# Performance work log

Hardware: AMD Instinct MI355X
Metric: run time of the kernel (lower is better)

Reference implementation:

```python
import jax, jax.numpy as jnp
import numpy as np

WIN = (9, 9)
EPS = float(np.power(np.e, -15))  # e^-15 threshold from original code


def _box_sum(x, win):
    kernel = jnp.ones((1, 1, win[0], win[1]), dtype=x.dtype)
    p = win[0] // 2
    return jax.lax.conv_general_dilated(
        x, kernel, window_strides=(1, 1), padding=[(p, p), (p, p)],
        dimension_numbers=("NCHW", "OIHW", "NCHW"))


def setup_inputs() -> dict:
    key = jax.random.key(0)
    k1, k2 = jax.random.split(key)
    B, C, H, W = 32, 1, 512, 512
    I = jax.random.normal(k1, (B, C, H, W), dtype=jnp.float32)
    J = jax.random.normal(k2, (B, C, H, W), dtype=jnp.float32)
    return {"I": I, "J": J}


def reference(I, J):
    win = WIN
    win_size = win[0] * win[1]
    I_sum = _box_sum(I, win)
    J_sum = _box_sum(J, win)
    I2_sum = _box_sum(I * I, win)
    J2_sum = _box_sum(J * J, win)
    IJ_sum = _box_sum(I * J, win)

    u_I = I_sum / win_size
    u_J = J_sum / win_size
    cross = IJ_sum - u_J * I_sum - u_I * J_sum + u_I * u_J * win_size
    I_var = I2_sum - 2 * u_I * I_sum + u_I * u_I * win_size
    J_var = J2_sum - 2 * u_J * J_sum + u_J * u_J * win_size

    non_zero = I_var * J_var > EPS
    cross = jnp.where(non_zero, cross, 1.0)
    I_var = jnp.where(non_zero, I_var, 1.0)
    J_var = jnp.where(non_zero, J_var, 1.0)

    cc = cross * cross / (I_var * J_var + EPS)
    return -1.0 * jnp.mean(cc, axis=(1, 2, 3)) + 1.0
```

## Files before the change

### kernel.cpp

```cpp
#include <hip/hip_runtime.h>


#define IMG_H 512
#define IMG_W 512
#define NBATCH 32
#define RPW 32
#define STRIPS_PER_IMG (IMG_H / RPW)
#define RING 10

typedef __attribute__((address_space(3))) void       lds_t;
typedef __attribute__((address_space(1))) const void glob_t;

__global__ __launch_bounds__(64, 1) void lcc_main(const float* __restrict__ I,
                                                  const float* __restrict__ J,
                                                  float* __restrict__ out) {
    __shared__ __align__(16) float ring[RING][1024];

    const int lane  = threadIdx.x;
    const int strip = blockIdx.x;
    const int b  = strip / STRIPS_PER_IMG;
    const int y0 = (strip % STRIPS_PER_IMG) * RPW;
    const int x0 = lane * 8;

    const float* __restrict__ Ib = I + (size_t)b * IMG_H * IMG_W;
    const float* __restrict__ Jb = J + (size_t)b * IMG_H * IMG_W;

    auto issue_row = [&](int y) {
        int slot = (y - y0 + 4) % RING;
        const float* gI = Ib + y * IMG_W;
        const float* gJ = Jb + y * IMG_W;
        float* lI = &ring[slot][0];
        float* lJ = &ring[slot][512];
        __builtin_amdgcn_global_load_lds((glob_t*)(gI +       lane * 4), (lds_t*)lI,         16, 0, 0);
        __builtin_amdgcn_global_load_lds((glob_t*)(gI + 256 + lane * 4), (lds_t*)(lI + 256), 16, 0, 0);
        __builtin_amdgcn_global_load_lds((glob_t*)(gJ +       lane * 4), (lds_t*)lJ,         16, 0, 0);
        __builtin_amdgcn_global_load_lds((glob_t*)(gJ + 256 + lane * 4), (lds_t*)(lJ + 256), 16, 0, 0);
    };

    float sI[8]  = {0.f,0.f,0.f,0.f,0.f,0.f,0.f,0.f};
    float sJ[8]  = {0.f,0.f,0.f,0.f,0.f,0.f,0.f,0.f};
    float sII[8] = {0.f,0.f,0.f,0.f,0.f,0.f,0.f,0.f};
    float sJJ[8] = {0.f,0.f,0.f,0.f,0.f,0.f,0.f,0.f};
    float sIJ[8] = {0.f,0.f,0.f,0.f,0.f,0.f,0.f,0.f};

    auto add_ld = [&](int y) {
        int slot = (y - y0 + 4) % RING;
        const float4* pI = reinterpret_cast<const float4*>(&ring[slot][x0]);
        const float4* pJ = reinterpret_cast<const float4*>(&ring[slot][512 + x0]);
        float4 i0 = pI[0], i1 = pI[1], j0 = pJ[0], j1 = pJ[1];
        float iv[8] = {i0.x,i0.y,i0.z,i0.w,i1.x,i1.y,i1.z,i1.w};
        float jv[8] = {j0.x,j0.y,j0.z,j0.w,j1.x,j1.y,j1.z,j1.w};
        #pragma unroll
        for (int c = 0; c < 8; ++c) {
            sI[c]  += iv[c];
            sJ[c]  += jv[c];
            sII[c]  = fmaf(iv[c], iv[c], sII[c]);
            sJJ[c]  = fmaf(jv[c], jv[c], sJJ[c]);
            sIJ[c]  = fmaf(iv[c], jv[c], sIJ[c]);
        }
    };
    auto sub_ld = [&](int y) {
        int slot = (y - y0 + 4) % RING;
        const float4* pI = reinterpret_cast<const float4*>(&ring[slot][x0]);
        const float4* pJ = reinterpret_cast<const float4*>(&ring[slot][512 + x0]);
        float4 i0 = pI[0], i1 = pI[1], j0 = pJ[0], j1 = pJ[1];
        float iv[8] = {i0.x,i0.y,i0.z,i0.w,i1.x,i1.y,i1.z,i1.w};
        float jv[8] = {j0.x,j0.y,j0.z,j0.w,j1.x,j1.y,j1.z,j1.w};
        #pragma unroll
        for (int c = 0; c < 8; ++c) {
            sI[c]  -= iv[c];
            sJ[c]  -= jv[c];
            sII[c]  = fmaf(-iv[c], iv[c], sII[c]);
            sJJ[c]  = fmaf(-jv[c], jv[c], sJJ[c]);
            sIJ[c]  = fmaf(-iv[c], jv[c], sIJ[c]);
        }
    };

    auto hsum = [&](const float (&s)[8], float (&h)[8]) {
        float w[16];
        #pragma unroll
        for (int c = 0; c < 8; ++c) w[4+c] = s[c];
        #pragma unroll
        for (int c = 0; c < 4; ++c) {
            float a = __shfl_up(s[4+c], 1);
            w[c] = lane ? a : 0.f;
            a = __shfl_down(s[c], 1);
            w[12+c] = (lane < 63) ? a : 0.f;
        }
        float acc = 0.f;
        #pragma unroll
        for (int i = 0; i < 9; ++i) acc += w[i];
        h[0] = acc;
        #pragma unroll
        for (int k = 1; k < 8; ++k) { acc += w[k+8] - w[k-1]; h[k] = acc; }
    };

    const int wy_lo = (y0 - 4 < 0) ? 0 : y0 - 4;
    const int wy_hi = y0 + 4;
    #pragma unroll 1
    for (int y = wy_lo; y <= wy_hi; ++y) issue_row(y);
    __builtin_amdgcn_s_waitcnt(0x3F70);
    #pragma unroll 1
    for (int y = wy_lo; y <= wy_hi; ++y) add_ld(y);

    const float inv81 = 1.0f / 81.0f;
    const float EPSV  = 3.0590232050182579e-07f;
    float local = 0.0f;

    #pragma unroll 1
    for (int r = 0; r < RPW; ++r) {
        const int t = y0 + r;

        const bool pf = (r + 1 < RPW) && (t + 5 < IMG_H);
        if (pf) {
            __builtin_amdgcn_s_waitcnt(0xC07F);
            issue_row(t + 5);
        }

        float hI[8], hJ[8], hII[8], hJJ[8], hIJ[8];
        hsum(sI,  hI);
        hsum(sJ,  hJ);
        hsum(sII, hII);
        hsum(sJJ, hJJ);
        hsum(sIJ, hIJ);

        #pragma unroll
        for (int k = 0; k < 8; ++k) {
            float cross = fmaf(hI[k] * hJ[k], -inv81, hIJ[k]);
            float Iv    = fmaf(hI[k] * hI[k], -inv81, hII[k]);
            float Jv    = fmaf(hJ[k] * hJ[k], -inv81, hJJ[k]);
            float p  = Iv * Jv;
            bool  nz = p > EPSV;
            float c2 = nz ? cross : 1.0f;
            float p2 = nz ? p : 1.0f;
            local += (c2 * c2) * __builtin_amdgcn_rcpf(p2 + EPSV);
        }

        if (r + 1 < RPW) {
            if (pf) __builtin_amdgcn_s_waitcnt(0x3F70);
            if (t + 5 < IMG_H) add_ld(t + 5);
            if (t - 4 >= 0)    sub_ld(t - 4);
        }
    }

    #pragma unroll
    for (int off = 32; off > 0; off >>= 1) local += __shfl_down(local, off);
    if (lane == 0)
        atomicAdd(out + b, fmaf(local, -1.0f / (float)(IMG_H * IMG_W),
                                1.0f / (float)STRIPS_PER_IMG));
}

extern "C" void kernel_launch(void* const* d_in, const int* in_sizes, int n_in,
                              void* d_out, int out_size, void* d_ws, size_t ws_size,
                              hipStream_t stream) {
    const float* I = (const float*)d_in[0];
    const float* J = (const float*)d_in[1];
    float* out = (float*)d_out;

    const int total_strips = NBATCH * STRIPS_PER_IMG;
    lcc_main<<<total_strips, 64, 0, stream>>>(I, J, out);
}
```

Before: 125.1 us.

## Replace LDS ring buffer with direct global loads and shorter strips

New measurement: 118.2 us. 1.06x faster.

```diff
diff --git a/kernel.cpp b/kernel.cpp
--- a/kernel.cpp
+++ b/kernel.cpp
@@ -4,18 +4,12 @@
 #define IMG_H 512
 #define IMG_W 512
 #define NBATCH 32
-#define RPW 32
+#define RPW 8
 #define STRIPS_PER_IMG (IMG_H / RPW)
-#define RING 10
 
-typedef __attribute__((address_space(3))) void       lds_t;
-typedef __attribute__((address_space(1))) const void glob_t;
-
-__global__ __launch_bounds__(64, 1) void lcc_main(const float* __restrict__ I,
+__global__ __launch_bounds__(64, 2) void lcc_main(const float* __restrict__ I,
                                                   const float* __restrict__ J,
                                                   float* __restrict__ out) {
-    __shared__ __align__(16) float ring[RING][1024];
-
     const int lane  = threadIdx.x;
     const int strip = blockIdx.x;
     const int b  = strip / STRIPS_PER_IMG;
@@ -25,16 +19,10 @@
     const float* __restrict__ Ib = I + (size_t)b * IMG_H * IMG_W;
     const float* __restrict__ Jb = J + (size_t)b * IMG_H * IMG_W;
 
-    auto issue_row = [&](int y) {
-        int slot = (y - y0 + 4) % RING;
-        const float* gI = Ib + y * IMG_W;
-        const float* gJ = Jb + y * IMG_W;
-        float* lI = &ring[slot][0];
-        float* lJ = &ring[slot][512];
-        __builtin_amdgcn_global_load_lds((glob_t*)(gI +       lane * 4), (lds_t*)lI,         16, 0, 0);
-        __builtin_amdgcn_global_load_lds((glob_t*)(gI + 256 + lane * 4), (lds_t*)(lI + 256), 16, 0, 0);
-        __builtin_amdgcn_global_load_lds((glob_t*)(gJ +       lane * 4), (lds_t*)lJ,         16, 0, 0);
-        __builtin_amdgcn_global_load_lds((glob_t*)(gJ + 256 + lane * 4), (lds_t*)(lJ + 256), 16, 0, 0);
+    auto load_row = [&](int y, float4& i0, float4& i1, float4& j0, float4& j1) {
+        const float4* pI = reinterpret_cast<const float4*>(Ib + (size_t)y * IMG_W + x0);
+        const float4* pJ = reinterpret_cast<const float4*>(Jb + (size_t)y * IMG_W + x0);
+        i0 = pI[0]; i1 = pI[1]; j0 = pJ[0]; j1 = pJ[1];
     };
 
     float sI[8]  = {0.f,0.f,0.f,0.f,0.f,0.f,0.f,0.f};
@@ -43,11 +31,8 @@
     float sJJ[8] = {0.f,0.f,0.f,0.f,0.f,0.f,0.f,0.f};
     float sIJ[8] = {0.f,0.f,0.f,0.f,0.f,0.f,0.f,0.f};
 
-    auto add_ld = [&](int y) {
-        int slot = (y - y0 + 4) % RING;
-        const float4* pI = reinterpret_cast<const float4*>(&ring[slot][x0]);
-        const float4* pJ = reinterpret_cast<const float4*>(&ring[slot][512 + x0]);
-        float4 i0 = pI[0], i1 = pI[1], j0 = pJ[0], j1 = pJ[1];
+    auto addv = [&](const float4& i0, const float4& i1,
+                    const float4& j0, const float4& j1) {
         float iv[8] = {i0.x,i0.y,i0.z,i0.w,i1.x,i1.y,i1.z,i1.w};
         float jv[8] = {j0.x,j0.y,j0.z,j0.w,j1.x,j1.y,j1.z,j1.w};
         #pragma unroll
@@ -59,11 +44,8 @@
             sIJ[c]  = fmaf(iv[c], jv[c], sIJ[c]);
         }
     };
-    auto sub_ld = [&](int y) {
-        int slot = (y - y0 + 4) % RING;
-        const float4* pI = reinterpret_cast<const float4*>(&ring[slot][x0]);
-        const float4* pJ = reinterpret_cast<const float4*>(&ring[slot][512 + x0]);
-        float4 i0 = pI[0], i1 = pI[1], j0 = pJ[0], j1 = pJ[1];
+    auto subv = [&](const float4& i0, const float4& i1,
+                    const float4& j0, const float4& j1) {
         float iv[8] = {i0.x,i0.y,i0.z,i0.w,i1.x,i1.y,i1.z,i1.w};
         float jv[8] = {j0.x,j0.y,j0.z,j0.w,j1.x,j1.y,j1.z,j1.w};
         #pragma unroll
@@ -95,13 +77,15 @@
         for (int k = 1; k < 8; ++k) { acc += w[k+8] - w[k-1]; h[k] = acc; }
     };
 
-    const int wy_lo = (y0 - 4 < 0) ? 0 : y0 - 4;
-    const int wy_hi = y0 + 4;
-    #pragma unroll 1
-    for (int y = wy_lo; y <= wy_hi; ++y) issue_row(y);
-    __builtin_amdgcn_s_waitcnt(0x3F70);
-    #pragma unroll 1
-    for (int y = wy_lo; y <= wy_hi; ++y) add_ld(y);
+    #pragma unroll
+    for (int k = 0; k < 9; ++k) {
+        const int y = y0 - 4 + k;
+        if (y >= 0) {
+            float4 i0, i1, j0, j1;
+            load_row(y, i0, i1, j0, j1);
+            addv(i0, i1, j0, j1);
+        }
+    }
 
     const float inv81 = 1.0f / 81.0f;
     const float EPSV  = 3.0590232050182579e-07f;
@@ -111,11 +95,12 @@
     for (int r = 0; r < RPW; ++r) {
         const int t = y0 + r;
 
-        const bool pf = (r + 1 < RPW) && (t + 5 < IMG_H);
-        if (pf) {
-            __builtin_amdgcn_s_waitcnt(0xC07F);
-            issue_row(t + 5);
-        }
+        const bool doadd = (r + 1 < RPW) && (t + 5 < IMG_H);
+        const bool dosub = (r + 1 < RPW) && (t - 4 >= 0);
+        float4 ai0 = {0,0,0,0}, ai1 = {0,0,0,0}, aj0 = {0,0,0,0}, aj1 = {0,0,0,0};
+        float4 bi0 = {0,0,0,0}, bi1 = {0,0,0,0}, bj0 = {0,0,0,0}, bj1 = {0,0,0,0};
+        if (doadd) load_row(t + 5, ai0, ai1, aj0, aj1);
+        if (dosub) load_row(t - 4, bi0, bi1, bj0, bj1);
 
         float hI[8], hJ[8], hII[8], hJJ[8], hIJ[8];
         hsum(sI,  hI);
@@ -136,11 +121,8 @@
             local += (c2 * c2) * __builtin_amdgcn_rcpf(p2 + EPSV);
         }
 
-        if (r + 1 < RPW) {
-            if (pf) __builtin_amdgcn_s_waitcnt(0x3F70);
-            if (t + 5 < IMG_H) add_ld(t + 5);
-            if (t - 4 >= 0)    sub_ld(t - 4);
-        }
+        if (doadd) addv(ai0, ai1, aj0, aj1);
+        if (dosub) subv(bi0, bi1, bj0, bj1);
     }
 
     #pragma unroll
```
